# Performance work log

Hardware: AMD Instinct MI355X
Metric: run time of the kernel (lower is better)

## Reference

```python
import jax, jax.numpy as jnp
import numpy as np

B, S, C, H = 2, 2048, 1024, 16
D = C // H  # head_size = 64


def setup_inputs() -> dict:
    key = jax.random.key(0)
    ks = jax.random.split(key, 8)
    scale = 1.0 / np.sqrt(C)
    return {
        "src": jax.random.normal(ks[0], (B, S, C), dtype=jnp.float32),
        "Wq": jax.random.normal(ks[1], (C, C), dtype=jnp.float32) * scale,
        "bq": jnp.zeros((C,), dtype=jnp.float32),
        "Wk": jax.random.normal(ks[2], (C, C), dtype=jnp.float32) * scale,
        "bk": jnp.zeros((C,), dtype=jnp.float32),
        "Wv": jax.random.normal(ks[3], (C, C), dtype=jnp.float32) * scale,
        "bv": jnp.zeros((C,), dtype=jnp.float32),
        "rel_k_table": jax.random.normal(ks[4], (2 * S - 1, D), dtype=jnp.float32),
    }


def reference(src, Wq, bq, Wk, bk, Wv, bv, rel_k_table):
    # Linear projections (torch Linear: x @ W.T + b)
    q = src @ Wq.T + bq  # (B,S,C)
    k = src @ Wk.T + bk
    v = src @ Wv.T + bv
    # Faithful to torch .view: raw reshape (B,S,C) -> (B,H,S,D), NOT a transpose split
    q = q.reshape(B, H, S, D)
    k = k.reshape(B, H, S, D)
    v = v.reshape(B, H, S, D)
    # content score: q @ k^T
    content = jnp.einsum("bhsd,bhtd->bhst", q, k)  # (B,H,S,S)
    # relative-position embeddings: (S,S,D)
    pos = jnp.arange(S)
    shifted = pos[None, :] - pos[:, None] + (S - 1)  # (S,S) in [0, 2S-2]
    rel_k = rel_k_table[shifted]  # (S,S,D)
    # q.view(S, B*H, D) @ rel_k.permute(0,2,1): batched over first (query-pos) axis
    q_r = q.reshape(S, B * H, D)
    pos_score = jnp.einsum("sbd,std->sbt", q_r, rel_k)  # (S,BH,S)
    pos_score = jnp.transpose(pos_score, (1, 0, 2)).reshape(B, H, S, S)
    scores = (content + pos_score) / jnp.sqrt(jnp.float32(D))
    attn = jax.nn.softmax(scores, axis=-1)
    out = jnp.einsum("bhst,bhtd->bhsd", attn, v)  # (B,H,S,D)
    out = jnp.transpose(out, (0, 2, 1, 3)).reshape(B, S, C)
    return out
```

## Files before the change

kernel.cpp:

```cpp
#include <hip/hip_runtime.h>
#include <hip/hip_bf16.h>

#define BATCH 2
#define SEQ   2048
#define CH    1024
#define NH    16
#define HD    64
#define BHN   (BATCH*NH)
#define SD    (SEQ*HD)

typedef short v8s __attribute__((ext_vector_type(8)));
typedef short v4s __attribute__((ext_vector_type(4)));
typedef float v4f __attribute__((ext_vector_type(4)));

__device__ __forceinline__ short f2bf(float f) {
    unsigned u = __float_as_uint(f);
    u += 0x7fff + ((u >> 16) & 1);
    return (short)(u >> 16);
}

__device__ __forceinline__ unsigned pk2bf(float a, float b) {
    __hip_bfloat162 h = __float22bfloat162_rn(make_float2(a, b));
    unsigned u;
    __builtin_memcpy(&u, &h, 4);
    return u;
}

__device__ __forceinline__ float ex2(float x) {
    float r; asm("v_exp_f32 %0, %1" : "=v"(r) : "v"(x)); return r;
}

#if __has_builtin(__builtin_amdgcn_perm)
#define PERMB(a, b, s) __builtin_amdgcn_perm((a), (b), (s))
#else
__device__ __forceinline__ unsigned PERMB(unsigned a, unsigned b, unsigned s) {
    unsigned r = 0;
#pragma unroll
    for (int i = 0; i < 4; i++) {
        unsigned sb = (s >> (8 * i)) & 0xff, byte;
        if (sb >= 12) byte = (sb == 12) ? 0u : 0xffu;
        else if (sb < 4) byte = (b >> (8 * sb)) & 0xff;
        else byte = (a >> (8 * (sb - 4))) & 0xff;
        r |= byte << (8 * i);
    }
    return r;
}
#endif

__device__ __forceinline__ void gl_lds16(const short* g, short* l) {
    __builtin_amdgcn_global_load_lds(
        (const __attribute__((address_space(1))) void*)g,
        (__attribute__((address_space(3))) void*)l, 16, 0, 0);
}

__global__ __launch_bounds__(256) void cast_all_kernel(
    const float* __restrict__ src, const float* __restrict__ wq,
    const float* __restrict__ wk, const float* __restrict__ wv,
    const float* __restrict__ rel,
    short* __restrict__ xb, short* __restrict__ wqb,
    short* __restrict__ wkb, short* __restrict__ wvb,
    short* __restrict__ relb)
{
    const int z = blockIdx.z;
    const float* s; short* d; int n4;
    switch (z) {
        case 0: s = src; d = xb;   n4 = 1048576; break;
        case 1: s = wq;  d = wqb;  n4 = 262144;  break;
        case 2: s = wk;  d = wkb;  n4 = 262144;  break;
        case 3: s = wv;  d = wvb;  n4 = 262144;  break;
        default: s = rel; d = relb; n4 = 65520;  break;
    }
    for (int i = blockIdx.x * 256 + threadIdx.x; i < n4; i += gridDim.x * 256) {
        float4 v = ((const float4*)s)[i];
        v4s o; o.x = f2bf(v.x); o.y = f2bf(v.y); o.z = f2bf(v.z); o.w = f2bf(v.w);
        ((v4s*)d)[i] = o;
    }
}

__global__ __launch_bounds__(256, 3) void proj_mfma_kernel(
    const short* __restrict__ Xb,
    const short* __restrict__ Wqb, const short* __restrict__ Wkb,
    const short* __restrict__ Wvb,
    const float* __restrict__ bq, const float* __restrict__ bk,
    const float* __restrict__ bv,
    short* __restrict__ qo, short* __restrict__ ko, short* __restrict__ vo)
{
    const int z = blockIdx.z;
    const short* W    = (z == 0) ? Wqb : (z == 1) ? Wkb : Wvb;
    const float* bias = (z == 0) ? bq  : (z == 1) ? bk  : bv;
    short*       out  = (z == 0) ? qo  : (z == 1) ? ko  : vo;
    const float  osc  = (z == 0) ? 0.125f * 1.44269504088896f : 1.0f;

    const int m0 = blockIdx.x * 128;
    const int n0 = blockIdx.y * 128;
    const int tid  = threadIdx.x;
    const int w    = tid >> 6;
    const int lane = tid & 63;
    const int l15  = lane & 15;
    const int quad = lane >> 4;
    const int wm = w & 1, wn = w >> 1;

    __shared__ short Al[128 * 32];
    __shared__ short Bl[128 * 32];

    v4f acc[4][4];
#pragma unroll
    for (int i = 0; i < 4; i++)
#pragma unroll
        for (int j = 0; j < 4; j++) acc[i][j] = (v4f)(0.f);

    const int lr = lane >> 2;
    const int lc = (lane & 3) * 8;

    for (int k0 = 0; k0 < 1024; k0 += 32) {
        __syncthreads();
#pragma unroll
        for (int l = 0; l < 2; l++) {
            const int slab = w * 32 + l * 16;
            gl_lds16(Xb + (size_t)(m0 + slab + lr) * 1024 + k0 + lc,
                     &Al[slab * 32]);
            gl_lds16(W + (size_t)(n0 + slab + lr) * 1024 + k0 + lc,
                     &Bl[slab * 32]);
        }
        __syncthreads();
        v8s af[4], bf[4];
#pragma unroll
        for (int mt = 0; mt < 4; mt++)
            af[mt] = *(const v8s*)&Al[(wm * 64 + mt * 16 + l15) * 32 + quad * 8];
#pragma unroll
        for (int nt = 0; nt < 4; nt++)
            bf[nt] = *(const v8s*)&Bl[(wn * 64 + nt * 16 + l15) * 32 + quad * 8];
#pragma unroll
        for (int mt = 0; mt < 4; mt++)
#pragma unroll
            for (int nt = 0; nt < 4; nt++)
                acc[mt][nt] = __builtin_amdgcn_mfma_f32_16x16x32_bf16(
                    af[mt], bf[nt], acc[mt][nt], 0, 0, 0);
    }

    float bv4[4];
#pragma unroll
    for (int nt = 0; nt < 4; nt++)
        bv4[nt] = bias[n0 + wn * 64 + nt * 16 + l15];
#pragma unroll
    for (int mt = 0; mt < 4; mt++)
#pragma unroll
        for (int rg = 0; rg < 4; rg++) {
            const int row = m0 + wm * 64 + mt * 16 + quad * 4 + rg;
#pragma unroll
            for (int nt = 0; nt < 4; nt++)
                out[(size_t)row * 1024 + n0 + wn * 64 + nt * 16 + l15] =
                    f2bf((acc[mt][nt][rg] + bv4[nt]) * osc);
        }
}

__global__ __launch_bounds__(256) void vtrans_kernel(
    const short* __restrict__ v, short* __restrict__ vt)
{
    const int bh = blockIdx.y;
    const int t0 = blockIdx.x * 64;
    const int r = threadIdx.x >> 3;
    const int c = (threadIdx.x & 7) * 8;

    __shared__ short T[64][72];
    *(v8s*)&T[r][c] =
        *(const v8s*)(v + (size_t)bh * SD + (size_t)(t0 + r) * HD + c);
    *(v8s*)&T[r + 32][c] =
        *(const v8s*)(v + (size_t)bh * SD + (size_t)(t0 + r + 32) * HD + c);
    __syncthreads();
    v8s o0, o1;
#pragma unroll
    for (int e = 0; e < 8; e++) {
        const int t = 2 * (threadIdx.x & 7) + (e >> 2) + 16 * (e & 3);
        o0[e] = T[t][r];
        o1[e] = T[t][r + 32];
    }
    *(v8s*)(vt + (size_t)bh * SD + (size_t)r * SEQ + t0 + c) = o0;
    *(v8s*)(vt + (size_t)bh * SD + (size_t)(r + 32) * SEQ + t0 + c) = o1;
}

__global__ __launch_bounds__(256, 2) void attn_mfma_kernel(
    const short* __restrict__ qb, const short* __restrict__ kb,
    const short* __restrict__ vtb, const short* __restrict__ relb,
    float* __restrict__ out)
{
    const int tid  = threadIdx.x;
    const int w    = tid >> 6;
    const int lane = tid & 63;
    const int l15  = lane & 15;
    const int quad = lane >> 4;
    const int bh = blockIdx.x, b = bh >> 4, h = bh & 15;
    const int s0 = blockIdx.y * 128;
    const int i0 = w * 32;

    __shared__ short Kl[2][64][64];
    __shared__ short Vl[2][64][64];
    __shared__ short Rl[256][64];
    __shared__ short Pb[4][2][16][64];

    v8s qc_f[2][2], qr_f[2][2];
#pragma unroll
    for (int mt = 0; mt < 2; mt++)
#pragma unroll
    for (int kh = 0; kh < 2; kh++) {
        const int row = s0 + i0 + mt * 16 + l15;
        qc_f[mt][kh] = *(const v8s*)(qb + (size_t)bh * SD +
                                     (size_t)row * HD + kh * 32 + quad * 8);
        qr_f[mt][kh] = *(const v8s*)(qb + (size_t)row * (BHN * HD) +
                                     bh * HD + kh * 32 + quad * 8);
    }

    int      slv4[4];
    unsigned selA[4], selB[4], pwoff[4];
#pragma unroll
    for (int rg = 0; rg < 4; rg++) {
        const int ii = quad * 4 + rg;
        const int e  = l15 + 15 - ii;
        const bool lo = (e < 16);
        slv4[rg] = (quad * 16 + (e & 15)) << 2;
        selA[rg] = lo ? 0x05040c0cu : 0x07060c0cu;
        selB[rg] = lo ? 0x07060c0cu : 0x01000c0cu;
        pwoff[rg] = (unsigned)(w * 4096 + ii * 128 +
                    ((((l15 >> 1) ^ (ii & 7)) << 4) + ((l15 & 1) << 3)));
    }

    const int swz = (quad ^ (l15 & 7)) << 4;
    int kaddr[2][4];
#pragma unroll
    for (int kh = 0; kh < 2; kh++) {
        const int x = kh << 6;
#pragma unroll
        for (int nt = 0; nt < 4; nt++)
            kaddr[kh][nt] = (((nt * 16 + l15) << 7) + swz) ^ x;
    }
    const int paddr0 = (l15 << 7) + swz;

    const int Bq = 1920 - s0;
    int raddr[6];
#pragma unroll
    for (int st = 0; st < 6; st++) {
        const int lg = 2032 - s0 - i0 - 16 + st * 16 + l15;
        raddr[st] = ((lg & 255) << 7) + ((quad ^ (lg & 7)) << 4);
    }

    const int strow = tid >> 3;
    const int stc   = ((tid & 7) ^ (strow & 7)) * 8;
    const short* ksrc = kb  + (size_t)bh * SD + (size_t)strow * HD  + stc;
    const short* vsrc = vtb + (size_t)bh * SD + (size_t)strow * SEQ + stc;

#pragma unroll
    for (int g = 0; g < 3; g++) {
        const int r0 = Bq + g * 64 + strow;
        const int ra = r0 < 4094 ? r0 : 4094;
        const int rb2 = (r0 + 32) < 4094 ? (r0 + 32) : 4094;
        const unsigned sl = (unsigned)((Bq + g * 64 + w * 8) & 255) << 7;
        gl_lds16(relb + (size_t)ra * HD + stc, (short*)((char*)Rl + sl));
        gl_lds16(relb + (size_t)rb2 * HD + stc, (short*)((char*)Rl + sl + 4096));
    }
    gl_lds16(ksrc,              &Kl[0][w * 8][0]);
    gl_lds16(ksrc + 32 * HD,    &Kl[0][32 + w * 8][0]);
    gl_lds16(vsrc,              &Vl[0][w * 8][0]);
    gl_lds16(vsrc + 32 * SEQ,   &Vl[0][32 + w * 8][0]);

    const short* kp = ksrc + 4096;
    const short* vp = vsrc + 64;
    const char*  relbp = (const char*)relb + stc * 2;
    unsigned roff = (unsigned)(Bq + 192 + strow) * 128;
    const unsigned ROMAX = 4094u * 128;
    unsigned rlds = (unsigned)((Bq + 192 + w * 8) & 255) << 7;

    v4f o_acc[2][4];
#pragma unroll
    for (int mt = 0; mt < 2; mt++)
#pragma unroll
        for (int nt = 0; nt < 4; nt++) o_acc[mt][nt] = (v4f)(0.f);
    float lpart[2][4] = {{0.f,0.f,0.f,0.f},{0.f,0.f,0.f,0.f}};

    int cur = 0;
    for (int t0 = 0; t0 < SEQ; t0 += 64, cur ^= 1) {
        __syncthreads();

        {
            const int nb = (cur ^ 1) << 12;
            short* kd = &Kl[0][w * 8][0] + nb;
            short* vd = &Vl[0][w * 8][0] + nb;
            gl_lds16(kp,            kd);
            gl_lds16(kp + 32 * HD,  kd + 32 * 64);
            gl_lds16(vp,            vd);
            gl_lds16(vp + 32 * SEQ, vd + 32 * 64);
            unsigned rc0 = roff < ROMAX ? roff : ROMAX;
            unsigned rc1 = (roff + 4096) < ROMAX ? (roff + 4096) : ROMAX;
            gl_lds16((const short*)(relbp + rc0), (short*)((char*)Rl + rlds));
            gl_lds16((const short*)(relbp + rc1), (short*)((char*)Rl + rlds + 4096));
        }
        kp += 4096; vp += 64; roff += 8192;
        rlds = (rlds + 8192) & 32767;

        v4f cacc[2][4], racc[2][5];
#pragma unroll
        for (int mt = 0; mt < 2; mt++) {
#pragma unroll
            for (int nt = 0; nt < 4; nt++) cacc[mt][nt] = (v4f)(0.f);
#pragma unroll
            for (int jt = 0; jt < 5; jt++) racc[mt][jt] = (v4f)(0.f);
        }

        const char* kbase = (const char*)Kl + cur * 8192;
        const char* vbase = (const char*)Vl + cur * 8192;
        const char* rbase = (const char*)Rl;

#pragma unroll
        for (int kh = 0; kh < 2; kh++) {
            v8s kf[4], rfj[6];
#pragma unroll
            for (int nt = 0; nt < 4; nt++)
                kf[nt] = *(const v8s*)(kbase + kaddr[kh][nt]);
#pragma unroll
            for (int st = 0; st < 6; st++)
                rfj[st] = *(const v8s*)(rbase + (raddr[st] ^ (kh << 6)));
            __builtin_amdgcn_s_setprio(1);
#pragma unroll
            for (int mt = 0; mt < 2; mt++)
#pragma unroll
                for (int nt = 0; nt < 4; nt++)
                    cacc[mt][nt] = __builtin_amdgcn_mfma_f32_16x16x32_bf16(
                        qc_f[mt][kh], kf[nt], cacc[mt][nt], 0, 0, 0);
#pragma unroll
            for (int jt = 0; jt < 5; jt++)
                racc[0][jt] = __builtin_amdgcn_mfma_f32_16x16x32_bf16(
                    qr_f[0][kh], rfj[jt + 1], racc[0][jt], 0, 0, 0);
#pragma unroll
            for (int jt = 0; jt < 5; jt++)
                racc[1][jt] = __builtin_amdgcn_mfma_f32_16x16x32_bf16(
                    qr_f[1][kh], rfj[jt], racc[1][jt], 0, 0, 0);
            __builtin_amdgcn_s_setprio(0);
        }
#pragma unroll
        for (int st = 0; st < 6; st++) raddr[st] = (raddr[st] + 8192) & 32767;

        unsigned g01[2][4], g23[2][4], g4v[2][4];
#pragma unroll
        for (int mt = 0; mt < 2; mt++)
#pragma unroll
        for (int rg = 0; rg < 4; rg++) {
            unsigned p01 = pk2bf(racc[mt][0][rg], racc[mt][1][rg]);
            unsigned p23 = pk2bf(racc[mt][2][rg], racc[mt][3][rg]);
            unsigned p4  = pk2bf(racc[mt][4][rg], racc[mt][4][rg]);
            g01[mt][rg] = (unsigned)__builtin_amdgcn_ds_bpermute(slv4[rg], (int)p01);
            g23[mt][rg] = (unsigned)__builtin_amdgcn_ds_bpermute(slv4[rg], (int)p23);
            g4v[mt][rg] = (unsigned)__builtin_amdgcn_ds_bpermute(slv4[rg], (int)p4);
        }
#pragma unroll
        for (int mt = 0; mt < 2; mt++)
#pragma unroll
        for (int rg = 0; rg < 4; rg++) {
            const unsigned a01 = g01[mt][rg], a23 = g23[mt][rg], a4 = g4v[mt][rg];
            unsigned pb0 = PERMB(a01, a01, selA[rg]);
            unsigned pb1 = PERMB(a01, a23, selB[rg]);
            unsigned pb2 = PERMB(a23, a23, selA[rg]);
            unsigned pb3 = PERMB(a23, a4,  selB[rg]);
            float p0 = ex2(cacc[mt][0][rg] + __uint_as_float(pb0));
            float p1 = ex2(cacc[mt][1][rg] + __uint_as_float(pb1));
            float p2 = ex2(cacc[mt][2][rg] + __uint_as_float(pb2));
            float p3 = ex2(cacc[mt][3][rg] + __uint_as_float(pb3));
            lpart[mt][rg] += (p0 + p1) + (p2 + p3);
            *(uint2*)((char*)Pb + pwoff[rg] + mt * 2048) =
                make_uint2(pk2bf(p0, p1), pk2bf(p2, p3));
        }

        const char* pbW = (const char*)Pb + w * 4096;
#pragma unroll
        for (int kh = 0; kh < 2; kh++) {
            v8s vf[4];
#pragma unroll
            for (int nt = 0; nt < 4; nt++)
                vf[nt] = *(const v8s*)(vbase + kaddr[kh][nt]);
            v8s pa0 = *(const v8s*)(pbW + (paddr0 ^ (kh << 6)));
            v8s pa1 = *(const v8s*)(pbW + 2048 + (paddr0 ^ (kh << 6)));
            __builtin_amdgcn_s_setprio(1);
#pragma unroll
            for (int nt = 0; nt < 4; nt++)
                o_acc[0][nt] = __builtin_amdgcn_mfma_f32_16x16x32_bf16(
                    pa0, vf[nt], o_acc[0][nt], 0, 0, 0);
#pragma unroll
            for (int nt = 0; nt < 4; nt++)
                o_acc[1][nt] = __builtin_amdgcn_mfma_f32_16x16x32_bf16(
                    pa1, vf[nt], o_acc[1][nt], 0, 0, 0);
            __builtin_amdgcn_s_setprio(0);
        }
    }

#pragma unroll
    for (int mt = 0; mt < 2; mt++)
#pragma unroll
    for (int rg = 0; rg < 4; rg++) {
        float rs = lpart[mt][rg];
#pragma unroll
        for (int off = 1; off < 16; off <<= 1)
            rs += __shfl_xor(rs, off);
        const float inv = 1.f / rs;
        const int row = s0 + i0 + mt * 16 + quad * 4 + rg;
        const size_t base = ((size_t)b * SEQ + row) * CH + h * HD;
#pragma unroll
        for (int nt = 0; nt < 4; nt++)
            out[base + nt * 16 + l15] = o_acc[mt][nt][rg] * inv;
    }
}

extern "C" void kernel_launch(void* const* d_in, const int* in_sizes, int n_in,
                              void* d_out, int out_size, void* d_ws, size_t ws_size,
                              hipStream_t stream)
{
    const float* src  = (const float*)d_in[0];
    const float* Wq   = (const float*)d_in[1];
    const float* bq   = (const float*)d_in[2];
    const float* Wk   = (const float*)d_in[3];
    const float* bk   = (const float*)d_in[4];
    const float* Wv   = (const float*)d_in[5];
    const float* bv   = (const float*)d_in[6];
    const float* relk = (const float*)d_in[7];
    float* out = (float*)d_out;

    const size_t nQKV = (size_t)BATCH * SEQ * CH;
    const size_t nW   = (size_t)CH * CH;
    short* qb   = (short*)d_ws;
    short* kb   = qb + nQKV;
    short* vb   = kb + nQKV;
    short* vtb  = vb + nQKV;
    short* xb   = vtb + nQKV;
    short* wqb  = xb + nQKV;
    short* wkb  = wqb + nW;
    short* wvb  = wkb + nW;
    short* relb = wvb + nW;

    cast_all_kernel<<<dim3(512, 1, 5), 256, 0, stream>>>(
        src, Wq, Wk, Wv, relk, xb, wqb, wkb, wvb, relb);

    dim3 gProj(4096 / 128, 1024 / 128, 3);
    proj_mfma_kernel<<<gProj, 256, 0, stream>>>(
        xb, wqb, wkb, wvb, bq, bk, bv, qb, kb, vb);

    dim3 gVt(SEQ / 64, BHN);
    vtrans_kernel<<<gVt, 256, 0, stream>>>(vb, vtb);

    dim3 gAttn(BHN, SEQ / 128);
    attn_mfma_kernel<<<gAttn, 256, 0, stream>>>(qb, kb, vtb, relb, out);
}
```

Baseline: 209.5 us.

## Software-pipeline attention loop so QK of next tile overlaps PV of previous

Result: no change. 208.7 us (-0.4%).

```diff
diff --git a/kernel.cpp b/kernel.cpp
--- a/kernel.cpp
+++ b/kernel.cpp
@@ -276,27 +276,10 @@
         for (int nt = 0; nt < 4; nt++) o_acc[mt][nt] = (v4f)(0.f);
     float lpart[2][4] = {{0.f,0.f,0.f,0.f},{0.f,0.f,0.f,0.f}};
 
-    int cur = 0;
-    for (int t0 = 0; t0 < SEQ; t0 += 64, cur ^= 1) {
-        __syncthreads();
-
-        {
-            const int nb = (cur ^ 1) << 12;
-            short* kd = &Kl[0][w * 8][0] + nb;
-            short* vd = &Vl[0][w * 8][0] + nb;
-            gl_lds16(kp,            kd);
-            gl_lds16(kp + 32 * HD,  kd + 32 * 64);
-            gl_lds16(vp,            vd);
-            gl_lds16(vp + 32 * SEQ, vd + 32 * 64);
-            unsigned rc0 = roff < ROMAX ? roff : ROMAX;
-            unsigned rc1 = (roff + 4096) < ROMAX ? (roff + 4096) : ROMAX;
-            gl_lds16((const short*)(relbp + rc0), (short*)((char*)Rl + rlds));
-            gl_lds16((const short*)(relbp + rc1), (short*)((char*)Rl + rlds + 4096));
-        }
-        kp += 4096; vp += 64; roff += 8192;
-        rlds = (rlds + 8192) & 32767;
-
-        v4f cacc[2][4], racc[2][5];
+    v4f cacc[2][4], racc[2][5];
+    unsigned g01[2][4], g23[2][4], g4v[2][4];
+
+    auto ZACC = [&]() {
 #pragma unroll
         for (int mt = 0; mt < 2; mt++) {
 #pragma unroll
@@ -304,11 +287,29 @@
 #pragma unroll
             for (int jt = 0; jt < 5; jt++) racc[mt][jt] = (v4f)(0.f);
         }
-
+    };
+
+    auto STAGE_K = [&](int dst) {
+        short* kd = &Kl[0][w * 8][0] + (dst << 12);
+        gl_lds16(kp,            kd);
+        gl_lds16(kp + 32 * HD,  kd + 32 * 64);
+        unsigned rc0 = roff < ROMAX ? roff : ROMAX;
+        unsigned rc1 = (roff + 4096) < ROMAX ? (roff + 4096) : ROMAX;
+        gl_lds16((const short*)(relbp + rc0), (short*)((char*)Rl + rlds));
+        gl_lds16((const short*)(relbp + rc1), (short*)((char*)Rl + rlds + 4096));
+        kp += 4096; roff += 8192; rlds = (rlds + 8192) & 32767;
+    };
+
+    auto STAGE_V = [&](int dst) {
+        short* vd = &Vl[0][w * 8][0] + (dst << 12);
+        gl_lds16(vp,            vd);
+        gl_lds16(vp + 32 * SEQ, vd + 32 * 64);
+        vp += 64;
+    };
+
+    auto QK = [&](int cur) {
         const char* kbase = (const char*)Kl + cur * 8192;
-        const char* vbase = (const char*)Vl + cur * 8192;
         const char* rbase = (const char*)Rl;
-
 #pragma unroll
         for (int kh = 0; kh < 2; kh++) {
             v8s kf[4], rfj[6];
@@ -337,8 +338,9 @@
         }
 #pragma unroll
         for (int st = 0; st < 6; st++) raddr[st] = (raddr[st] + 8192) & 32767;
-
-        unsigned g01[2][4], g23[2][4], g4v[2][4];
+    };
+
+    auto PHASE1 = [&]() {
 #pragma unroll
         for (int mt = 0; mt < 2; mt++)
 #pragma unroll
@@ -350,6 +352,9 @@
             g23[mt][rg] = (unsigned)__builtin_amdgcn_ds_bpermute(slv4[rg], (int)p23);
             g4v[mt][rg] = (unsigned)__builtin_amdgcn_ds_bpermute(slv4[rg], (int)p4);
         }
+    };
+
+    auto PHASE2 = [&]() {
 #pragma unroll
         for (int mt = 0; mt < 2; mt++)
 #pragma unroll
@@ -367,7 +372,10 @@
             *(uint2*)((char*)Pb + pwoff[rg] + mt * 2048) =
                 make_uint2(pk2bf(p0, p1), pk2bf(p2, p3));
         }
-
+    };
+
+    auto PV = [&](int vbuf) {
+        const char* vbase = (const char*)Vl + vbuf * 8192;
         const char* pbW = (const char*)Pb + w * 4096;
 #pragma unroll
         for (int kh = 0; kh < 2; kh++) {
@@ -388,7 +396,26 @@
                     pa1, vf[nt], o_acc[1][nt], 0, 0, 0);
             __builtin_amdgcn_s_setprio(0);
         }
-    }
+    };
+
+    __syncthreads();
+    STAGE_K(1);
+    STAGE_V(1);
+    ZACC(); QK(0); PHASE1(); PHASE2();
+
+    int cur = 0;
+    for (int t0 = 64; t0 < SEQ; t0 += 64) {
+        cur ^= 1;
+        __syncthreads();
+        STAGE_K(cur ^ 1);
+        ZACC(); QK(cur);
+        PHASE1();
+        PV(cur ^ 1);
+        __syncthreads();
+        STAGE_V(cur ^ 1);
+        PHASE2();
+    }
+    PV(cur);
 
 #pragma unroll
     for (int mt = 0; mt < 2; mt++)
```
